# Performance work log

Hardware: AMD Instinct MI355X
Metric: run time of the kernel (lower is better)

The kernel has to match this reference:

```python
import jax, jax.numpy as jnp
import numpy as np

C_IN, C_OUT = 64, 32
SD, RFF = 2, 16
RF = 0.05          # receptive_field percentile
TEMP = 1.0
EPS = 1e-8
RFF_STD = 6.0


def setup_inputs() -> dict:
    key = jax.random.key(0)
    ks = jax.random.split(key, 10)
    B_, T, V, Q = 2, 4, 2048, 512
    x = jax.random.normal(ks[0], (B_, T, V, C_IN), dtype=jnp.float32)
    pos = jax.random.uniform(ks[1], (V, SD), dtype=jnp.float32)
    query_pos = jax.random.uniform(ks[2], (Q, SD), dtype=jnp.float32)
    s = 1.0 / np.sqrt(C_IN)
    W_lin = jax.random.uniform(ks[3], (C_IN, C_IN), minval=-s, maxval=s, dtype=jnp.float32)
    b_lin = jax.random.uniform(ks[4], (C_IN,), minval=-s, maxval=s, dtype=jnp.float32)
    Bmat = RFF_STD * jax.random.normal(ks[5], (SD, RFF), dtype=jnp.float32)
    s1 = 1.0 / np.sqrt(32)
    W1 = jax.random.uniform(ks[6], (32, 32), minval=-s1, maxval=s1, dtype=jnp.float32)
    b1 = jax.random.uniform(ks[7], (32,), minval=-s1, maxval=s1, dtype=jnp.float32)
    W2 = jax.random.uniform(ks[8], (C_IN * C_OUT, 32), minval=-s1, maxval=s1, dtype=jnp.float32)
    sf = np.sqrt(3.0 / C_IN)
    filt = jax.random.uniform(ks[9], (C_IN * C_OUT,), minval=-sf, maxval=sf, dtype=jnp.float32)
    bias = jnp.zeros((C_OUT,), dtype=jnp.float32)
    return {"x": x, "pos": pos, "query_pos": query_pos, "W_lin": W_lin, "b_lin": b_lin,
            "Bmat": Bmat, "W1": W1, "b1": b1, "W2": W2, "filt": filt, "bias": bias}


def reference(x, pos, query_pos, W_lin, b_lin, Bmat, W1, b1, W2, filt, bias):
    # pairwise periodic displacement / squared distance
    dist = query_pos[:, None, :] - pos[None, :, :]            # (Q, V, 2)
    dist = (dist + 0.5) % 1.0 - 0.5                           # periodic wrap
    edist = jnp.sum(dist ** 2, axis=-1)                       # (Q, V)
    # quantile threshold -> max neighbourhood size (eager, data-dependent like torch)
    thr = jnp.quantile(edist, RF, axis=-1, keepdims=True)     # linear interpolation, as torch
    K = int(jnp.max(jnp.sum(edist <= thr, axis=-1)))
    _, ind = jax.lax.top_k(-edist, K)                         # (Q, K) nearest neighbours
    # gather per-query neighbour displacements / distances
    d_g = jnp.take_along_axis(dist, ind[..., None], axis=1)   # (Q, K, 2)
    e_g = jnp.take_along_axis(edist, ind, axis=1)[..., None]  # (Q, K, 1)
    e_g = e_g - jnp.min(e_g, axis=-2, keepdims=True)
    e_g = e_g / (jnp.max(e_g, axis=-2, keepdims=True) + EPS)
    k_dist = jax.nn.softmax(-e_g / TEMP, axis=-2)             # (Q, K, 1)
    # random Fourier features + kernel MLP
    proj = 2.0 * jnp.pi * (d_g @ Bmat)                        # (Q, K, 16)
    kfeat = jnp.concatenate([jnp.sin(proj), jnp.cos(proj)], axis=-1)  # (Q, K, 32)
    h = jax.nn.gelu(kfeat @ W1.T + b1, approximate=False)
    ker = (h @ W2.T + filt) * k_dist                          # (Q, K, C_IN*C_OUT)
    ker = ker.reshape(ker.shape[0], ker.shape[1], C_IN, C_OUT)
    # point-wise linear on features, then gather + contract
    xl = x @ W_lin.T + b_lin                                  # (B, T, V, C_IN)
    xg = xl[:, :, ind, :]                                     # (B, T, Q, K, C_IN)
    return jnp.einsum('qvcd,btqvc->btqd', ker, xg) + bias     # (B, T, Q, C_OUT)
```

## Files before the change

### kernel.cpp

```cpp
#include <hip/hip_runtime.h>

#define K_SEL 103
typedef unsigned long long ull_t;
typedef _Float16 f16x8 __attribute__((ext_vector_type(8)));
typedef float f32x4 __attribute__((ext_vector_type(4)));

__global__ __launch_bounds__(512, 6) void k12(const float* __restrict__ pos,
                                              const float* __restrict__ qpos,
                                              const float* __restrict__ Bmat,
                                              const float* __restrict__ W1,
                                              const float* __restrict__ b1,
                                              _Float16* __restrict__ Hh,
                                              int* __restrict__ indg,
                                              float* __restrict__ invtot,
                                              const float* __restrict__ x,
                                              const float* __restrict__ W,
                                              const float* __restrict__ b,
                                              _Float16* __restrict__ xlh,
                                              const float* __restrict__ W2,
                                              const float* __restrict__ filt,
                                              _Float16* __restrict__ W2th) {
    __shared__ __align__(16) unsigned char smem[30880];
    const int tid = threadIdx.x;
    const int bid = blockIdx.x;
    const int lane = tid & 63;
    const int wid = tid >> 6;

    if (bid >= 512) {
        const int bb = bid - 512;
        float* Wt = (float*)smem;
        if (tid < 264) {
            int t = bb * 264 + tid;
            int d = t & 31;
            int e = t >> 5;
            int c = e & 63;
            int j = e >> 6;
            float v = (j < 32) ? W2[(c * 32 + d) * 32 + j] : filt[c * 32 + d];
            W2th[d * 2112 + e] = (_Float16)v;
        }
        for (int t = tid; t < 4096; t += 512)
            Wt[(t & 63) * 65 + (t >> 6)] = W[t];
        __syncthreads();
        const int i = tid & 63;
        const int sub = tid >> 6;
        const float bi = b[i];
        #pragma unroll
        for (int rr = 0; rr < 2; ++rr) {
            const int r0 = bb * 64 + rr * 32 + sub * 4;
            float acc0 = bi, acc1 = bi, acc2 = bi, acc3 = bi;
            const float* xr = x + (size_t)r0 * 64;
            #pragma unroll 4
            for (int jj = 0; jj < 16; ++jj) {
                float4 v0 = *(const float4*)(xr + 0 * 64 + jj * 4);
                float4 v1 = *(const float4*)(xr + 1 * 64 + jj * 4);
                float4 v2 = *(const float4*)(xr + 2 * 64 + jj * 4);
                float4 v3 = *(const float4*)(xr + 3 * 64 + jj * 4);
                float w0 = Wt[(jj * 4 + 0) * 65 + i];
                float w1 = Wt[(jj * 4 + 1) * 65 + i];
                float w2 = Wt[(jj * 4 + 2) * 65 + i];
                float w3 = Wt[(jj * 4 + 3) * 65 + i];
                acc0 += v0.x * w0 + v0.y * w1 + v0.z * w2 + v0.w * w3;
                acc1 += v1.x * w0 + v1.y * w1 + v1.z * w2 + v1.w * w3;
                acc2 += v2.x * w0 + v2.y * w1 + v2.z * w2 + v2.w * w3;
                acc3 += v3.x * w0 + v3.y * w1 + v3.z * w2 + v3.w * w3;
            }
            xlh[(size_t)(r0 + 0) * 64 + i] = (_Float16)acc0;
            xlh[(size_t)(r0 + 1) * 64 + i] = (_Float16)acc1;
            xlh[(size_t)(r0 + 2) * 64 + i] = (_Float16)acc2;
            xlh[(size_t)(r0 + 3) * 64 + i] = (_Float16)acc3;
        }
        return;
    }

    const int q = bid;
    unsigned* ebits   = (unsigned*)(smem);
    unsigned* hist    = (unsigned*)(smem + 8192);
    _Float16* Hs      = (_Float16*)(smem + 8192);
    float*    W1s     = (float*)(smem + 24576);
    float*    b1s     = (float*)(smem + 28672);
    float*    Bm      = (float*)(smem + 28800);
    int*      sel_v   = (int*)(smem + 28928);
    float*    sel_e   = (float*)(smem + 29344);
    ull_t*    bnd     = (ull_t*)(smem + 29760);
    int*      counters= (int*)(smem + 30784);
    int*      info    = (int*)(smem + 30792);
    float*    wred    = (float*)(smem + 30800);
    float*    emax_s  = (float*)(smem + 30832);
    unsigned* wscan   = (unsigned*)(smem + 30836);

    for (int t = tid; t < 1024; t += 512) W1s[t] = W1[t];
    if (tid < 32) { b1s[tid] = b1[tid]; Bm[tid] = Bmat[tid]; }
    if (tid < 2)  counters[tid] = 0;
    for (int t = tid; t < 1024; t += 512) ((uint4*)hist)[t] = make_uint4(0, 0, 0, 0);
    const float qp0 = qpos[q * 2 + 0];
    const float qp1 = qpos[q * 2 + 1];
    __syncthreads();

    float lmin = 1e30f;
    for (int v = tid; v < 2048; v += 512) {
        float2 p = ((const float2*)pos)[v];
        float d0 = qp0 - p.x;
        float d1 = qp1 - p.y;
        d0 += 0.5f; d0 -= floorf(d0); d0 -= 0.5f;
        d1 += 0.5f; d1 -= floorf(d1); d1 -= 0.5f;
        float e = d0 * d0 + d1 * d1;
        ebits[v] = __float_as_uint(e);
        lmin = fminf(lmin, e);
        int bb2 = (int)(e * 8192.0f); bb2 = (bb2 > 4095) ? 4095 : bb2;
        atomicAdd(&hist[bb2], 1u);
    }
    #pragma unroll
    for (int off = 32; off > 0; off >>= 1)
        lmin = fminf(lmin, __shfl_xor(lmin, off, 64));
    if (lane == 0) wred[wid] = lmin;
    __syncthreads();
    float e_min = wred[0];
    #pragma unroll
    for (int w2 = 1; w2 < 8; ++w2) e_min = fminf(e_min, wred[w2]);

    unsigned lsum = 0;
    #pragma unroll
    for (int i = 0; i < 8; ++i) lsum += hist[tid * 8 + i];
    unsigned vq = lsum;
    #pragma unroll
    for (int off = 1; off < 64; off <<= 1) {
        unsigned n = __shfl_up(vq, off, 64);
        if (lane >= off) vq += n;
    }
    if (lane == 63) wscan[wid] = vq;
    __syncthreads();
    unsigned base = 0;
    for (int w2 = 0; w2 < wid; ++w2) base += wscan[w2];
    unsigned cum = base + vq - lsum;
    #pragma unroll
    for (int i = 0; i < 8; ++i) {
        unsigned cnt = hist[tid * 8 + i];
        if (cum <= 102u && 102u < cum + cnt) { info[0] = tid * 8 + i; info[1] = (int)cum; }
        cum += cnt;
    }
    __syncthreads();
    const int Bstar = info[0];
    const int L = info[1];
    const int need = K_SEL - L;

    {
        f16x8 z = {0, 0, 0, 0, 0, 0, 0, 0};
        for (int t = tid; t < 768; t += 512) ((f16x8*)Hs)[t] = z;
    }
    for (int v = tid; v < 2048; v += 512) {
        unsigned bb2 = ebits[v];
        float e = __uint_as_float(bb2);
        int bin = (int)(e * 8192.0f); bin = (bin > 4095) ? 4095 : bin;
        if (bin < Bstar) {
            int s2 = atomicAdd(&counters[0], 1);
            sel_v[s2] = v; sel_e[s2] = e;
        } else if (bin == Bstar) {
            int s2 = atomicAdd(&counters[1], 1);
            if (s2 < 128) bnd[s2] = (((ull_t)bb2) << 32) | (unsigned)v;
        }
    }
    __syncthreads();
    if (tid == 0) {
        int nb = counters[1]; if (nb > 128) nb = 128;
        for (int i = 1; i < nb; ++i) {
            ull_t key = bnd[i]; int j2 = i - 1;
            while (j2 >= 0 && bnd[j2] > key) { bnd[j2 + 1] = bnd[j2]; --j2; }
            bnd[j2 + 1] = key;
        }
        for (int i = 0; i < need; ++i) {
            sel_v[L + i] = (int)(unsigned)(bnd[i] & 0xffffffffull);
            sel_e[L + i] = __uint_as_float((unsigned)(bnd[i] >> 32));
        }
        emax_s[0] = __uint_as_float((unsigned)(bnd[need - 1] >> 32));
    }
    __syncthreads();

    const float denom = (emax_s[0] - e_min) + 1e-8f;
    float w = 0.0f;
    if (tid < K_SEL) {
        w = __expf(-(sel_e[tid] - e_min) / denom);
        sel_e[tid] = w;
    }
    float sw = w;
    #pragma unroll
    for (int off = 32; off > 0; off >>= 1)
        sw += __shfl_xor(sw, off, 64);
    if (lane == 0) wred[wid] = sw;
    __syncthreads();
    if (tid == 0) {
        float tot = 0.0f;
        #pragma unroll
        for (int w2 = 0; w2 < 8; ++w2) tot += wred[w2];
        invtot[q] = 1.0f / tot;
    }

    if (tid < 4 * K_SEL) {
        const int k = tid >> 2;
        const int io = (tid & 3) * 8;
        const int v = sel_v[k];
        const float wk = sel_e[k];
        float2 p = ((const float2*)pos)[v];
        float d0 = qp0 - p.x;
        float d1 = qp1 - p.y;
        d0 += 0.5f; d0 -= floorf(d0); d0 -= 0.5f;
        d1 += 0.5f; d1 -= floorf(d1); d1 -= 0.5f;
        float kf[32];
        #pragma unroll
        for (int f = 0; f < 16; ++f) {
            float t = d0 * Bm[f] + d1 * Bm[16 + f];
            float r = t - rintf(t);
            kf[f]      = __builtin_amdgcn_sinf(r);
            kf[16 + f] = __builtin_amdgcn_cosf(r);
        }
        #pragma unroll
        for (int i = io; i < io + 8; ++i) {
            float pre = b1s[i];
            #pragma unroll
            for (int jf = 0; jf < 32; ++jf) pre += kf[jf] * W1s[i * 32 + jf];
            float g = 0.5f * pre * (1.0f + erff(pre * 0.70710678118654752f));
            Hs[i * 128 + k] = (_Float16)(g * wk);
        }
        if (io == 0) {
            Hs[32 * 128 + k] = (_Float16)wk;
            indg[q * K_SEL + k] = v;
        }
    }
    __syncthreads();
    {
        _Float16* hq = Hh + (size_t)q * 6144;
        for (int t = tid; t < 768; t += 512)
            ((f16x8*)hq)[t] = ((const f16x8*)Hs)[t];
    }
}

__global__ __launch_bounds__(256, 4) void k3_main(const _Float16* __restrict__ xlh,
                                                  const _Float16* __restrict__ Hh,
                                                  const int* __restrict__ indg,
                                                  const _Float16* __restrict__ W2th,
                                                  const float* __restrict__ bias,
                                                  const float* __restrict__ invtot,
                                                  float* __restrict__ out) {
    const int bid = blockIdx.x;
    const int q = bid >> 1;
    const int bt0 = (bid & 1) * 4;
    const int tid = threadIdx.x;
    const int lane = tid & 63;
    const int wv = tid >> 6;
    const int n0 = lane & 15;
    const int quad = lane >> 4;

    __shared__ __align__(16) unsigned char smem[34944];
    _Float16* Xg  = (_Float16*)smem;
    _Float16* Zh4 = (_Float16*)(smem + 17536);
    int* ind_s    = (int*)(smem + 34432);
    float* red    = (float*)smem;

    const _Float16* hq = Hh + (size_t)q * 6144;
    f16x8 afr[4][3];
    #pragma unroll
    for (int ks = 0; ks < 4; ++ks)
        #pragma unroll
        for (int r = 0; r < 3; ++r)
            afr[ks][r] = *(const f16x8*)(hq + (r * 16 + n0) * 128 + ks * 32 + quad * 8);
    const float it = invtot[q];
    const int e0f = wv * 32 + quad * 8;
    f16x8 pf0 = *(const f16x8*)(W2th + (size_t)(0 * 16 + n0) * 2112 + e0f);
    f16x8 pf1 = *(const f16x8*)(W2th + (size_t)(1 * 16 + n0) * 2112 + e0f);
    if (tid < 128) {
        int kk = (tid < K_SEL) ? tid : tid - K_SEL;
        ind_s[tid] = indg[q * K_SEL + kk];
    }
    __syncthreads();

    int g_k[4], g_oct[4];
    #pragma unroll
    for (int i = 0; i < 4; ++i) {
        int t = tid + i * 256;
        g_k[i] = t >> 3;
        g_oct[i] = t & 7;
    }

    {
        f16x8 v0[4];
        #pragma unroll
        for (int i = 0; i < 4; ++i)
            v0[i] = *(const f16x8*)(xlh + ((size_t)bt0 * 2048 + ind_s[g_k[i]]) * 64 + g_oct[i] * 8);
        #pragma unroll
        for (int i = 0; i < 4; ++i) {
            int base = g_oct[i] * 1096 + g_k[i];
            #pragma unroll
            for (int jj = 0; jj < 8; ++jj) Xg[base + 136 * jj] = v0[i][jj];
        }
    }
    __syncthreads();

    const int cA = wv * 16 + n0;
    const int cswz = cA * 136 + ((cA >> 3) << 3);

    #pragma unroll
    for (int p = 0; p < 4; ++p) {
        f16x8 vn[4];
        if (p < 3) {
            #pragma unroll
            for (int i = 0; i < 4; ++i)
                vn[i] = *(const f16x8*)(xlh + ((size_t)(bt0 + p + 1) * 2048 + ind_s[g_k[i]]) * 64 + g_oct[i] * 8);
        }
        f32x4 Dz[3];
        #pragma unroll
        for (int r = 0; r < 3; ++r) Dz[r] = (f32x4){0.f, 0.f, 0.f, 0.f};
        #pragma unroll
        for (int ks = 0; ks < 4; ++ks) {
            f16x8 bfr = *(const f16x8*)(&Xg[cswz + ks * 32 + quad * 8]);
            #pragma unroll
            for (int r = 0; r < 3; ++r)
                Dz[r] = __builtin_amdgcn_mfma_f32_16x16x32_f16(afr[ks][r], bfr, Dz[r], 0, 0, 0);
        }
        __syncthreads();
        #pragma unroll
        for (int r = 0; r < 3; ++r)
            #pragma unroll
            for (int reg = 0; reg < 4; ++reg) {
                int j = r * 16 + quad * 4 + reg;
                if (j < 33) Zh4[p * 2112 + j * 64 + cA] = (_Float16)Dz[r][reg];
            }
        if (p < 3) {
            #pragma unroll
            for (int i = 0; i < 4; ++i) {
                int base = g_oct[i] * 1096 + g_k[i];
                #pragma unroll
                for (int jj = 0; jj < 8; ++jj) Xg[base + 136 * jj] = vn[i][jj];
            }
            __syncthreads();
        }
    }
    __syncthreads();

    f32x4 D2[2][2];
    #pragma unroll
    for (int pp = 0; pp < 2; ++pp)
        #pragma unroll
        for (int dt = 0; dt < 2; ++dt) D2[pp][dt] = (f32x4){0.f, 0.f, 0.f, 0.f};
    {
        f16x8 a2 = {0, 0, 0, 0, 0, 0, 0, 0};
        if (n0 < 4) a2 = *(const f16x8*)(&Zh4[n0 * 2112 + e0f]);
        D2[0][0] = __builtin_amdgcn_mfma_f32_16x16x32_f16(a2, pf0, D2[0][0], 0, 0, 0);
        D2[0][1] = __builtin_amdgcn_mfma_f32_16x16x32_f16(a2, pf1, D2[0][1], 0, 0, 0);
    }
    int pp = 1;
    #pragma unroll 2
    for (int s = wv + 4; s < 66; s += 4) {
        const int e0 = s * 32 + quad * 8;
        f16x8 a2 = {0, 0, 0, 0, 0, 0, 0, 0};
        if (n0 < 4) a2 = *(const f16x8*)(&Zh4[n0 * 2112 + e0]);
        #pragma unroll
        for (int dt = 0; dt < 2; ++dt) {
            f16x8 bfr = *(const f16x8*)(W2th + (size_t)(dt * 16 + n0) * 2112 + e0);
            D2[pp][dt] = __builtin_amdgcn_mfma_f32_16x16x32_f16(a2, bfr, D2[pp][dt], 0, 0, 0);
        }
        pp ^= 1;
    }
    #pragma unroll
    for (int dt = 0; dt < 2; ++dt)
        D2[0][dt] = D2[0][dt] + D2[1][dt];

    if (quad == 0) {
        #pragma unroll
        for (int dt = 0; dt < 2; ++dt)
            #pragma unroll
            for (int reg = 0; reg < 4; ++reg)
                red[((wv * 2 + dt) * 4 + reg) * 16 + n0] = D2[0][dt][reg];
    }
    __syncthreads();
    if (tid < 128) {
        const int bt = tid >> 5;
        const int d = tid & 31;
        const int dt = d >> 4;
        const int dn = d & 15;
        float s = 0.0f;
        #pragma unroll
        for (int w2 = 0; w2 < 4; ++w2)
            s += red[((w2 * 2 + dt) * 4 + bt) * 16 + dn];
        out[((size_t)(bt0 + bt) * 512 + q) * 32 + d] = bias[d] + it * s;
    }
}

extern "C" void kernel_launch(void* const* d_in, const int* in_sizes, int n_in,
                              void* d_out, int out_size, void* d_ws, size_t ws_size,
                              hipStream_t stream) {
    const float* x     = (const float*)d_in[0];
    const float* pos   = (const float*)d_in[1];
    const float* qpos  = (const float*)d_in[2];
    const float* W_lin = (const float*)d_in[3];
    const float* b_lin = (const float*)d_in[4];
    const float* Bmat  = (const float*)d_in[5];
    const float* W1    = (const float*)d_in[6];
    const float* b1    = (const float*)d_in[7];
    const float* W2    = (const float*)d_in[8];
    const float* filt  = (const float*)d_in[9];
    const float* bias  = (const float*)d_in[10];
    float* out = (float*)d_out;

    float* ws = (float*)d_ws;
    _Float16* xlh    = (_Float16*)ws;
    _Float16* Hh     = (_Float16*)(ws + 524288);
    int*      indg   = (int*)(ws + 2097152);
    _Float16* W2th   = (_Float16*)(ws + 2150144);
    float*    invtot = ws + 2183936;

    k12<<<768, 512, 0, stream>>>(pos, qpos, Bmat, W1, b1, Hh, indg, invtot,
                                 x, W_lin, b_lin, xlh, W2, filt, W2th);
    k3_main<<<1024, 256, 0, stream>>>(xlh, Hh, indg, W2th, bias, invtot, out);
}
```

Before: 120.6 us.

## Process all eight batch-time slices per query in one 512-thread block

k3_main now assigns one block per query covering all 8 (B,T) slices, with two wave halves each taking one slice per step. Previously two 256-thread blocks per query each handled 4 slices. The change means each per-query H fragment and index list is loaded once instead of twice. The second-stage GEMM now fills 8 rows of the MFMA A operand instead of 4, so each W2th fragment load serves twice as many rows. The cost is larger LDS use (about 69 KB per block), which may lower occupancy, and half as many blocks in the grid.

```diff
diff --git a/kernel.cpp b/kernel.cpp
--- a/kernel.cpp
+++ b/kernel.cpp
@@ -233,26 +233,26 @@
     }
 }
 
-__global__ __launch_bounds__(256, 4) void k3_main(const _Float16* __restrict__ xlh,
+__global__ __launch_bounds__(512, 4) void k3_main(const _Float16* __restrict__ xlh,
                                                   const _Float16* __restrict__ Hh,
                                                   const int* __restrict__ indg,
                                                   const _Float16* __restrict__ W2th,
                                                   const float* __restrict__ bias,
                                                   const float* __restrict__ invtot,
                                                   float* __restrict__ out) {
-    const int bid = blockIdx.x;
-    const int q = bid >> 1;
-    const int bt0 = (bid & 1) * 4;
+    const int q = blockIdx.x;
     const int tid = threadIdx.x;
     const int lane = tid & 63;
-    const int wv = tid >> 6;
+    const int wid = tid >> 6;
+    const int h   = wid >> 2;
+    const int cq  = wid & 3;
     const int n0 = lane & 15;
     const int quad = lane >> 4;
 
-    __shared__ __align__(16) unsigned char smem[34944];
+    __shared__ __align__(16) unsigned char smem[69376];
     _Float16* Xg  = (_Float16*)smem;
-    _Float16* Zh4 = (_Float16*)(smem + 17536);
-    int* ind_s    = (int*)(smem + 34432);
+    _Float16* Zh8 = (_Float16*)(smem + 35072);
+    int* ind_s    = (int*)(smem + 68864);
     float* red    = (float*)smem;
 
     const _Float16* hq = Hh + (size_t)q * 6144;
@@ -263,7 +263,7 @@
         for (int r = 0; r < 3; ++r)
             afr[ks][r] = *(const f16x8*)(hq + (r * 16 + n0) * 128 + ks * 32 + quad * 8);
     const float it = invtot[q];
-    const int e0f = wv * 32 + quad * 8;
+    const int e0f = wid * 32 + quad * 8;
     f16x8 pf0 = *(const f16x8*)(W2th + (size_t)(0 * 16 + n0) * 2112 + e0f);
     f16x8 pf1 = *(const f16x8*)(W2th + (size_t)(1 * 16 + n0) * 2112 + e0f);
     if (tid < 128) {
@@ -272,11 +272,12 @@
     }
     __syncthreads();
 
-    int g_k[4], g_oct[4];
+    int g_k[4], g_oct[4], g_h[4];
     #pragma unroll
     for (int i = 0; i < 4; ++i) {
-        int t = tid + i * 256;
-        g_k[i] = t >> 3;
+        int t = tid + i * 512;
+        g_h[i] = t >> 10;
+        g_k[i] = (t >> 3) & 127;
         g_oct[i] = t & 7;
     }
 
@@ -284,18 +285,18 @@
         f16x8 v0[4];
         #pragma unroll
         for (int i = 0; i < 4; ++i)
-            v0[i] = *(const f16x8*)(xlh + ((size_t)bt0 * 2048 + ind_s[g_k[i]]) * 64 + g_oct[i] * 8);
+            v0[i] = *(const f16x8*)(xlh + ((size_t)g_h[i] * 2048 + ind_s[g_k[i]]) * 64 + g_oct[i] * 8);
         #pragma unroll
         for (int i = 0; i < 4; ++i) {
-            int base = g_oct[i] * 1096 + g_k[i];
+            int base = g_h[i] * 8768 + g_oct[i] * 1096 + g_k[i];
             #pragma unroll
             for (int jj = 0; jj < 8; ++jj) Xg[base + 136 * jj] = v0[i][jj];
         }
     }
     __syncthreads();
 
-    const int cA = wv * 16 + n0;
-    const int cswz = cA * 136 + ((cA >> 3) << 3);
+    const int cA = cq * 16 + n0;
+    const int cswz = h * 8768 + cA * 136 + ((cA >> 3) << 3);
 
     #pragma unroll
     for (int p = 0; p < 4; ++p) {
@@ -303,7 +304,7 @@
         if (p < 3) {
             #pragma unroll
             for (int i = 0; i < 4; ++i)
-                vn[i] = *(const f16x8*)(xlh + ((size_t)(bt0 + p + 1) * 2048 + ind_s[g_k[i]]) * 64 + g_oct[i] * 8);
+                vn[i] = *(const f16x8*)(xlh + ((size_t)(2 * (p + 1) + g_h[i]) * 2048 + ind_s[g_k[i]]) * 64 + g_oct[i] * 8);
         }
         f32x4 Dz[3];
         #pragma unroll
@@ -316,17 +317,18 @@
                 Dz[r] = __builtin_amdgcn_mfma_f32_16x16x32_f16(afr[ks][r], bfr, Dz[r], 0, 0, 0);
         }
         __syncthreads();
+        const int bt = 2 * p + h;
         #pragma unroll
         for (int r = 0; r < 3; ++r)
             #pragma unroll
             for (int reg = 0; reg < 4; ++reg) {
                 int j = r * 16 + quad * 4 + reg;
-                if (j < 33) Zh4[p * 2112 + j * 64 + cA] = (_Float16)Dz[r][reg];
+                if (j < 33) Zh8[bt * 2112 + j * 64 + cA] = (_Float16)Dz[r][reg];
             }
         if (p < 3) {
             #pragma unroll
             for (int i = 0; i < 4; ++i) {
-                int base = g_oct[i] * 1096 + g_k[i];
+                int base = g_h[i] * 8768 + g_oct[i] * 1096 + g_k[i];
                 #pragma unroll
                 for (int jj = 0; jj < 8; ++jj) Xg[base + 136 * jj] = vn[i][jj];
             }
@@ -342,16 +344,16 @@
         for (int dt = 0; dt < 2; ++dt) D2[pp][dt] = (f32x4){0.f, 0.f, 0.f, 0.f};
     {
         f16x8 a2 = {0, 0, 0, 0, 0, 0, 0, 0};
-        if (n0 < 4) a2 = *(const f16x8*)(&Zh4[n0 * 2112 + e0f]);
+        if (n0 < 8) a2 = *(const f16x8*)(&Zh8[n0 * 2112 + e0f]);
         D2[0][0] = __builtin_amdgcn_mfma_f32_16x16x32_f16(a2, pf0, D2[0][0], 0, 0, 0);
         D2[0][1] = __builtin_amdgcn_mfma_f32_16x16x32_f16(a2, pf1, D2[0][1], 0, 0, 0);
     }
     int pp = 1;
     #pragma unroll 2
-    for (int s = wv + 4; s < 66; s += 4) {
+    for (int s = wid + 8; s < 66; s += 8) {
         const int e0 = s * 32 + quad * 8;
         f16x8 a2 = {0, 0, 0, 0, 0, 0, 0, 0};
-        if (n0 < 4) a2 = *(const f16x8*)(&Zh4[n0 * 2112 + e0]);
+        if (n0 < 8) a2 = *(const f16x8*)(&Zh8[n0 * 2112 + e0]);
         #pragma unroll
         for (int dt = 0; dt < 2; ++dt) {
             f16x8 bfr = *(const f16x8*)(W2th + (size_t)(dt * 16 + n0) * 2112 + e0);
@@ -363,24 +365,24 @@
     for (int dt = 0; dt < 2; ++dt)
         D2[0][dt] = D2[0][dt] + D2[1][dt];
 
-    if (quad == 0) {
+    if (quad < 2) {
         #pragma unroll
         for (int dt = 0; dt < 2; ++dt)
             #pragma unroll
             for (int reg = 0; reg < 4; ++reg)
-                red[((wv * 2 + dt) * 4 + reg) * 16 + n0] = D2[0][dt][reg];
-    }
-    __syncthreads();
-    if (tid < 128) {
+                red[((wid * 2 + dt) * 8 + quad * 4 + reg) * 16 + n0] = D2[0][dt][reg];
+    }
+    __syncthreads();
+    if (tid < 256) {
         const int bt = tid >> 5;
         const int d = tid & 31;
         const int dt = d >> 4;
         const int dn = d & 15;
         float s = 0.0f;
         #pragma unroll
-        for (int w2 = 0; w2 < 4; ++w2)
-            s += red[((w2 * 2 + dt) * 4 + bt) * 16 + dn];
-        out[((size_t)(bt0 + bt) * 512 + q) * 32 + d] = bias[d] + it * s;
+        for (int w2 = 0; w2 < 8; ++w2)
+            s += red[((w2 * 2 + dt) * 8 + bt) * 16 + dn];
+        out[((size_t)bt * 512 + q) * 32 + d] = bias[d] + it * s;
     }
 }
 
@@ -409,5 +411,5 @@
 
     k12<<<768, 512, 0, stream>>>(pos, qpos, Bmat, W1, b1, Hh, indg, invtot,
                                  x, W_lin, b_lin, xlh, W2, filt, W2th);
-    k3_main<<<1024, 256, 0, stream>>>(xlh, Hh, indg, W2th, bias, invtot, out);
+    k3_main<<<512, 512, 0, stream>>>(xlh, Hh, indg, W2th, bias, invtot, out);
 }
```

New measurement: 112.3 us. 1.07x faster.
